# Performance work log

Hardware: AMD Instinct MI355X
Metric: run time of the kernel (lower is better)

## Reference

```python
import jax, jax.numpy as jnp
import numpy as np

NEG_INF = -1e6

def setup_inputs() -> dict:
    key = jax.random.key(0)
    ks = jax.random.split(key, 7)
    B, Q, K, D, H = 16, 64, 1024, 256, 128
    return {
        "queries": jax.random.normal(ks[0], (B, Q, D), dtype=jnp.float32),
        "keys": jax.random.normal(ks[1], (B, K, D), dtype=jnp.float32),
        "values": jax.random.normal(ks[2], (B, K, D), dtype=jnp.float32),
        "valid_lens": jax.random.randint(ks[3], (B,), 1, K + 1, dtype=jnp.int32),
        "W_q": jax.random.normal(ks[4], (D, H), dtype=jnp.float32) * (1.0 / np.sqrt(D)),
        "W_k": jax.random.normal(ks[5], (D, H), dtype=jnp.float32) * (1.0 / np.sqrt(D)),
        "w_v": jax.random.normal(ks[6], (H,), dtype=jnp.float32) * (1.0 / np.sqrt(H)),
    }

def reference(queries, keys, values, valid_lens, W_q, W_k, w_v):
    # project: [B,Q,H], [B,K,H]
    q = jnp.einsum('bqd,dh->bqh', queries, W_q)
    k = jnp.einsum('bkd,dh->bkh', keys, W_k)
    # broadcast add -> tanh -> score: [B,Q,K]
    features = jnp.tanh(q[:, :, None, :] + k[:, None, :, :])  # [B,Q,K,H]
    scores = jnp.einsum('bqkh,h->bqk', features, w_v)
    # masked softmax over key axis (valid_lens per batch)
    K_len = keys.shape[1]
    mask = jnp.arange(K_len)[None, None, :] < valid_lens[:, None, None]  # [B,1,K]
    scores = jnp.where(mask, scores, NEG_INF)
    attn = jax.nn.softmax(scores, axis=-1)
    # weighted sum of values: [B,Q,Dv]  (dropout p=0 -> identity)
    return jnp.einsum('bqk,bkd->bqd', attn, values)
```

## Files before the change

kernel.cpp:

```cpp
#include <hip/hip_runtime.h>

#define DDIM 256
#define HDIM 128
#define KLEN 1024
#define SCL 2.8853900817779268f

__global__ __launch_bounds__(256) void proj_kernel(
    const float* __restrict__ queries, const float* __restrict__ keys,
    const float* __restrict__ W_q, const float* __restrict__ W_k,
    float* __restrict__ Eq, float* __restrict__ Ek)
{
    __shared__ union {
        float a[64 * 64];
        float t[32][68];
    } sm;

    const int tid  = threadIdx.x;
    const int lane = tid & 63;
    const int wav  = tid >> 6;

    int blk = blockIdx.x;
    bool iskey; int b = 0, kc0 = 0, hb, row0;
    const float* in; const float* W;
    if (blk < 1024) {
        iskey = true;
        int xcd = blk & 7, s = blk >> 3;
        b = ((s >> 6) << 3) | xcd;
        int r6 = s & 63;
        kc0 = (r6 >> 2) << 6;
        hb  = (r6 & 3) << 5;
        row0 = b * KLEN + kc0;
        in = keys; W = W_k;
    } else {
        iskey = false;
        int qrb = blk - 1024;
        row0 = (qrb >> 2) << 6;
        hb   = (qrb & 3) << 5;
        in = queries; W = W_q;
    }

    const int hg8 = __builtin_amdgcn_readfirstlane(wav << 3);
    const float* Wu = W + hb + hg8;

    const int srow = tid >> 4;
    const int sgd  = tid & 15;
    const float* gsrc = in + (size_t)(row0 + srow) * DDIM + (sgd << 2);

    float4 pf0 = *(const float4*)(gsrc);
    float4 pf1 = *(const float4*)(gsrc + 16 * DDIM);
    float4 pf2 = *(const float4*)(gsrc + 32 * DDIM);
    float4 pf3 = *(const float4*)(gsrc + 48 * DDIM);

    float acc[8];
    #pragma unroll
    for (int c = 0; c < 8; c++) acc[c] = 0.f;

    const int w0 = (srow)      * 64 + ((sgd ^ ((srow)      & 7)) << 2);
    const int w1 = (srow + 16) * 64 + ((sgd ^ ((srow + 16) & 7)) << 2);
    const int w2 = (srow + 32) * 64 + ((sgd ^ ((srow + 32) & 7)) << 2);
    const int w3 = (srow + 48) * 64 + ((sgd ^ ((srow + 48) & 7)) << 2);

    for (int dt0 = 0; dt0 < DDIM; dt0 += 64) {
        *(float4*)(sm.a + w0) = pf0;
        *(float4*)(sm.a + w1) = pf1;
        *(float4*)(sm.a + w2) = pf2;
        *(float4*)(sm.a + w3) = pf3;
        __syncthreads();
        if (dt0 < DDIM - 64) {
            const float* g2 = gsrc + dt0 + 64;
            pf0 = *(const float4*)(g2);
            pf1 = *(const float4*)(g2 + 16 * DDIM);
            pf2 = *(const float4*)(g2 + 32 * DDIM);
            pf3 = *(const float4*)(g2 + 48 * DDIM);
        }
        const float* arow = sm.a + lane * 64;
        const int lx = lane & 7;
        #pragma unroll
        for (int d4 = 0; d4 < 64; d4 += 4) {
            float4 a = *(const float4*)(arow + ((((d4 >> 2)) ^ lx) << 2));
            const float* wr = Wu + (size_t)(dt0 + d4) * HDIM;
            #pragma unroll
            for (int c = 0; c < 8; c++) acc[c] = fmaf(a.x, wr[c],            acc[c]);
            #pragma unroll
            for (int c = 0; c < 8; c++) acc[c] = fmaf(a.y, wr[HDIM + c],     acc[c]);
            #pragma unroll
            for (int c = 0; c < 8; c++) acc[c] = fmaf(a.z, wr[2 * HDIM + c], acc[c]);
            #pragma unroll
            for (int c = 0; c < 8; c++) acc[c] = fmaf(a.w, wr[3 * HDIM + c], acc[c]);
        }
        __syncthreads();
    }

    float e[8];
    #pragma unroll
    for (int c = 0; c < 8; c++) e[c] = __builtin_amdgcn_exp2f(SCL * acc[c]);

    if (!iskey) {
        float* dst = Eq + (size_t)(row0 + lane) * HDIM + hb + hg8;
        *(float4*)(dst)     = make_float4(e[0], e[1], e[2], e[3]);
        *(float4*)(dst + 4) = make_float4(e[4], e[5], e[6], e[7]);
    } else {
        #pragma unroll
        for (int c = 0; c < 8; c++) sm.t[(wav << 3) + c][lane] = e[c];
        __syncthreads();
        float* dstb = Ek + (size_t)b * HDIM * KLEN + (size_t)hb * KLEN + kc0;
        #pragma unroll
        for (int i = 0; i < 2; i++) {
            int g = tid + (i << 8);
            int h = g >> 4, k4 = (g & 15) << 2;
            float4 o = *(const float4*)(&sm.t[h][k4]);
            *(float4*)(dstb + (size_t)h * KLEN + k4) = o;
        }
    }
}

__global__ __launch_bounds__(256) void score_kernel(
    const float* __restrict__ Eq, const float* __restrict__ Ek,
    const float* __restrict__ w_v, const int* __restrict__ valid_lens,
    float* __restrict__ E)
{
    __shared__ float ekt[16][128];
    __shared__ float eqs[8][HDIM];
    __shared__ float w2s[HDIM];

    const int tid = threadIdx.x;
    const int lane = tid & 63, wav = tid >> 6;
    int blk = blockIdx.x;
    int xcd = blk & 7, s = blk >> 3;
    int b = ((s >> 6) << 3) | xcd;
    int r = s & 63;
    int qt = r >> 3, kq = r & 7;
    int bq0 = b * 64 + qt * 8;
    int k0g = kq << 7;

    if (tid < HDIM) w2s[tid] = -2.0f * w_v[tid];
    #pragma unroll
    for (int i = 0; i < 4; i++) {
        int slot = tid + (i << 8);
        int q = slot >> 7, h = slot & 127;
        eqs[q][h] = Eq[(size_t)(bq0 + q) * HDIM + h];
    }

    const float* ekb = Ek + (size_t)b * HDIM * KLEN + k0g;
    float4 pf[2];
    #pragma unroll
    for (int i = 0; i < 2; i++) {
        int slot = tid + (i << 8);
        int row = slot >> 5, g = slot & 31;
        pf[i] = *(const float4*)(ekb + (size_t)row * KLEN + (g << 2));
    }

    const int q0 = wav << 1;
    const int kl = lane << 1;
    float2 acc[2] = {make_float2(0.f, 0.f), make_float2(0.f, 0.f)};

    for (int c = 0; c < 8; c++) {
        __syncthreads();
        #pragma unroll
        for (int i = 0; i < 2; i++) {
            int slot = tid + (i << 8);
            int row = slot >> 5, g = slot & 31;
            *(float4*)(&ekt[row][g << 2]) = pf[i];
        }
        __syncthreads();
        if (c < 7) {
            const float* nx = ekb + (size_t)((c + 1) << 4) * KLEN;
            #pragma unroll
            for (int i = 0; i < 2; i++) {
                int slot = tid + (i << 8);
                int row = slot >> 5, g = slot & 31;
                pf[i] = *(const float4*)(nx + (size_t)row * KLEN + (g << 2));
            }
        }
        const int c16 = c << 4;
        #pragma unroll
        for (int h4 = 0; h4 < 16; h4 += 4) {
            float4 eqa = *(const float4*)(&eqs[q0][c16 + h4]);
            float4 eqb = *(const float4*)(&eqs[q0 + 1][c16 + h4]);
            float4 w2v = *(const float4*)(&w2s[c16 + h4]);
            float ea[4] = {eqa.x, eqa.y, eqa.z, eqa.w};
            float eb[4] = {eqb.x, eqb.y, eqb.z, eqb.w};
            float wv[4] = {w2v.x, w2v.y, w2v.z, w2v.w};
            #pragma unroll
            for (int hh = 0; hh < 4; hh++) {
                float2 ek = *(const float2*)(&ekt[h4 + hh][kl]);
                float w2 = wv[hh];
                acc[0].x = fmaf(w2, __builtin_amdgcn_rcpf(fmaf(ea[hh], ek.x, 1.f)), acc[0].x);
                acc[0].y = fmaf(w2, __builtin_amdgcn_rcpf(fmaf(ea[hh], ek.y, 1.f)), acc[0].y);
                acc[1].x = fmaf(w2, __builtin_amdgcn_rcpf(fmaf(eb[hh], ek.x, 1.f)), acc[1].x);
                acc[1].y = fmaf(w2, __builtin_amdgcn_rcpf(fmaf(eb[hh], ek.y, 1.f)), acc[1].y);
            }
        }
    }

    int vlen = valid_lens[b];
    int kg = k0g + kl;
    #pragma unroll
    for (int j = 0; j < 2; j++) {
        float2 ev;
        ev.x = (kg     < vlen) ? __expf(acc[j].x) : 0.f;
        ev.y = (kg + 1 < vlen) ? __expf(acc[j].y) : 0.f;
        *(float2*)(E + (size_t)(bq0 + q0 + j) * KLEN + kg) = ev;
    }
}

__global__ __launch_bounds__(256) void av_kernel(
    const float* __restrict__ E, const float* __restrict__ values,
    const int* __restrict__ valid_lens, float* __restrict__ part,
    float* __restrict__ Tp)
{
    __shared__ union {
        float  pt[512][8];
        float4 slab[4][8][64];
    } sm;
    __shared__ float tslab[4][8];

    int blk = blockIdx.x;
    int xcd = blk & 7, s = blk >> 3;
    int b = ((s >> 4) << 3) | xcd;
    int r = s & 15, qt = r >> 1, kh = r & 1;
    int tid = threadIdx.x, lane = tid & 63, w = tid >> 6;
    int vlen = valid_lens[b];
    int bq0 = b * 64 + qt * 8;
    int kbase = kh << 9;

    #pragma unroll
    for (int i = 0; i < 4; i++) {
        int slot = tid + (i << 8);
        int q = slot >> 7, k4 = (slot & 127) << 2;
        float4 pv = *(const float4*)(E + (size_t)(bq0 + q) * KLEN + kbase + k4);
        sm.pt[k4 + 0][q] = pv.x;
        sm.pt[k4 + 1][q] = pv.y;
        sm.pt[k4 + 2][q] = pv.z;
        sm.pt[k4 + 3][q] = pv.w;
    }
    __syncthreads();

    int kw = w << 7;
    int cnt = vlen - (kbase + kw); cnt = cnt < 0 ? 0 : (cnt > 128 ? 128 : cnt);
    int cnt4 = (cnt + 3) & ~3;
    const float* vb = values + ((size_t)b * KLEN + kbase + kw) * DDIM + (lane << 2);

    float4 acc[8];
    float acct[8];
    #pragma unroll
    for (int q = 0; q < 8; q++) { acc[q] = make_float4(0.f, 0.f, 0.f, 0.f); acct[q] = 0.f; }

    for (int k = 0; k < cnt4; k += 4) {
        #pragma unroll
        for (int j = 0; j < 4; j++) {
            float4 v  = *(const float4*)(vb + (size_t)(k + j) * DDIM);
            float4 p0 = *(const float4*)(&sm.pt[kw + k + j][0]);
            float4 p1 = *(const float4*)(&sm.pt[kw + k + j][4]);
            float pq[8] = {p0.x, p0.y, p0.z, p0.w, p1.x, p1.y, p1.z, p1.w};
            #pragma unroll
            for (int q = 0; q < 8; q++) {
                acc[q].x = fmaf(pq[q], v.x, acc[q].x);
                acc[q].y = fmaf(pq[q], v.y, acc[q].y);
                acc[q].z = fmaf(pq[q], v.z, acc[q].z);
                acc[q].w = fmaf(pq[q], v.w, acc[q].w);
                acct[q] += pq[q];
            }
        }
    }

    __syncthreads();
    #pragma unroll
    for (int q = 0; q < 8; q++) sm.slab[w][q][lane] = acc[q];
    if (lane == 0) {
        #pragma unroll
        for (int q = 0; q < 8; q++) tslab[w][q] = acct[q];
    }
    __syncthreads();
    #pragma unroll
    for (int e = 0; e < 2; e++) {
        int slot = (tid << 1) | e;
        int q = slot >> 6, d4 = slot & 63;
        float4 a = sm.slab[0][q][d4];
        #pragma unroll
        for (int g = 1; g < 4; g++) {
            float4 t = sm.slab[g][q][d4];
            a.x += t.x; a.y += t.y; a.z += t.z; a.w += t.w;
        }
        *(float4*)(part + ((size_t)kh * 1024 + bq0 + q) * DDIM + (d4 << 2)) = a;
    }
    if (tid < 8) {
        float t = tslab[0][tid] + tslab[1][tid] + tslab[2][tid] + tslab[3][tid];
        Tp[(size_t)kh * 1024 + bq0 + tid] = t;
    }
}

__global__ __launch_bounds__(256) void combine_kernel(
    const float* __restrict__ part, const float* __restrict__ Tp,
    float* __restrict__ out)
{
    int i = blockIdx.x * 256 + threadIdx.x;
    int row = i >> 6;
    const float4* p4 = (const float4*)part;
    float4 a = p4[i];
    float4 v = p4[65536 + i];
    float inv = 1.0f / (Tp[row] + Tp[1024 + row]);
    a.x = (a.x + v.x) * inv; a.y = (a.y + v.y) * inv;
    a.z = (a.z + v.z) * inv; a.w = (a.w + v.w) * inv;
    ((float4*)out)[i] = a;
}

extern "C" void kernel_launch(void* const* d_in, const int* in_sizes, int n_in,
                              void* d_out, int out_size, void* d_ws, size_t ws_size,
                              hipStream_t stream) {
    const float* queries    = (const float*)d_in[0];
    const float* keys       = (const float*)d_in[1];
    const float* values     = (const float*)d_in[2];
    const int*   valid_lens = (const int*)d_in[3];
    const float* W_q        = (const float*)d_in[4];
    const float* W_k        = (const float*)d_in[5];
    const float* w_v        = (const float*)d_in[6];

    float* Eq   = (float*)d_ws;
    float* Ek   = Eq + 131072;
    float* E    = Ek + 2097152;
    float* Tp   = E + 1048576;
    float* part = Ek;

    proj_kernel<<<1088, 256, 0, stream>>>(queries, keys, W_q, W_k, Eq, Ek);
    score_kernel<<<1024, 256, 0, stream>>>(Eq, Ek, w_v, valid_lens, E);
    av_kernel<<<256, 256, 0, stream>>>(E, values, valid_lens, part, Tp);
    combine_kernel<<<256, 256, 0, stream>>>(part, Tp, (float*)d_out);
}
```

Baseline: 154.7 us.

## Fuse score and attention-value kernels, split key axis into eight partials

Merges the score kernel and the AV kernel into one kernel. Each block computes exp-scores for its 8 queries × 128 keys, keeps them in shared memory, and immediately accumulates the weighted values for that key chunk. This removes the global round trip of the score matrix E and one kernel launch. Ek is now read straight from global memory through a register double buffer instead of being staged in shared memory. The split-K factor grows from 2 to 8, so the combine kernel now reduces 8 partial outputs and 8 partial sums, which adds partial-buffer traffic.

```diff
diff --git a/kernel.cpp b/kernel.cpp
--- a/kernel.cpp
+++ b/kernel.cpp
@@ -114,14 +114,20 @@
     }
 }
 
-__global__ __launch_bounds__(256) void score_kernel(
+__global__ __launch_bounds__(256) void score_av_kernel(
     const float* __restrict__ Eq, const float* __restrict__ Ek,
     const float* __restrict__ w_v, const int* __restrict__ valid_lens,
-    float* __restrict__ E)
+    const float* __restrict__ values,
+    float* __restrict__ part, float* __restrict__ Tp)
 {
-    __shared__ float ekt[16][128];
-    __shared__ float eqs[8][HDIM];
-    __shared__ float w2s[HDIM];
+    __shared__ union {
+        struct {
+            float4 eqw[4][HDIM];
+            float  el[128][8];
+        } p;
+        float4 slab[4][8][64];
+    } sm;
+    __shared__ float tslab[4][8];
 
     const int tid = threadIdx.x;
     const int lane = tid & 63, wav = tid >> 6;
@@ -132,114 +138,63 @@
     int qt = r >> 3, kq = r & 7;
     int bq0 = b * 64 + qt * 8;
     int k0g = kq << 7;
-
-    if (tid < HDIM) w2s[tid] = -2.0f * w_v[tid];
-    #pragma unroll
-    for (int i = 0; i < 4; i++) {
-        int slot = tid + (i << 8);
-        int q = slot >> 7, h = slot & 127;
-        eqs[q][h] = Eq[(size_t)(bq0 + q) * HDIM + h];
-    }
-
-    const float* ekb = Ek + (size_t)b * HDIM * KLEN + k0g;
-    float4 pf[2];
+    int vlen = valid_lens[b];
+
     #pragma unroll
     for (int i = 0; i < 2; i++) {
         int slot = tid + (i << 8);
-        int row = slot >> 5, g = slot & 31;
-        pf[i] = *(const float4*)(ekb + (size_t)row * KLEN + (g << 2));
-    }
-
-    const int q0 = wav << 1;
+        int w = slot >> 7, h = slot & 127;
+        sm.p.eqw[w][h] = make_float4(
+            Eq[(size_t)(bq0 + 2 * w) * HDIM + h],
+            Eq[(size_t)(bq0 + 2 * w + 1) * HDIM + h],
+            -2.0f * w_v[h], 0.f);
+    }
+    __syncthreads();
+
     const int kl = lane << 1;
-    float2 acc[2] = {make_float2(0.f, 0.f), make_float2(0.f, 0.f)};
-
-    for (int c = 0; c < 8; c++) {
-        __syncthreads();
-        #pragma unroll
-        for (int i = 0; i < 2; i++) {
-            int slot = tid + (i << 8);
-            int row = slot >> 5, g = slot & 31;
-            *(float4*)(&ekt[row][g << 2]) = pf[i];
-        }
-        __syncthreads();
-        if (c < 7) {
-            const float* nx = ekb + (size_t)((c + 1) << 4) * KLEN;
-            #pragma unroll
-            for (int i = 0; i < 2; i++) {
-                int slot = tid + (i << 8);
-                int row = slot >> 5, g = slot & 31;
-                pf[i] = *(const float4*)(nx + (size_t)row * KLEN + (g << 2));
-            }
-        }
-        const int c16 = c << 4;
-        #pragma unroll
-        for (int h4 = 0; h4 < 16; h4 += 4) {
-            float4 eqa = *(const float4*)(&eqs[q0][c16 + h4]);
-            float4 eqb = *(const float4*)(&eqs[q0 + 1][c16 + h4]);
-            float4 w2v = *(const float4*)(&w2s[c16 + h4]);
-            float ea[4] = {eqa.x, eqa.y, eqa.z, eqa.w};
-            float eb[4] = {eqb.x, eqb.y, eqb.z, eqb.w};
-            float wv[4] = {w2v.x, w2v.y, w2v.z, w2v.w};
-            #pragma unroll
-            for (int hh = 0; hh < 4; hh++) {
-                float2 ek = *(const float2*)(&ekt[h4 + hh][kl]);
-                float w2 = wv[hh];
-                acc[0].x = fmaf(w2, __builtin_amdgcn_rcpf(fmaf(ea[hh], ek.x, 1.f)), acc[0].x);
-                acc[0].y = fmaf(w2, __builtin_amdgcn_rcpf(fmaf(ea[hh], ek.y, 1.f)), acc[0].y);
-                acc[1].x = fmaf(w2, __builtin_amdgcn_rcpf(fmaf(eb[hh], ek.x, 1.f)), acc[1].x);
-                acc[1].y = fmaf(w2, __builtin_amdgcn_rcpf(fmaf(eb[hh], ek.y, 1.f)), acc[1].y);
-            }
-        }
-    }
-
-    int vlen = valid_lens[b];
-    int kg = k0g + kl;
-    #pragma unroll
-    for (int j = 0; j < 2; j++) {
-        float2 ev;
-        ev.x = (kg     < vlen) ? __expf(acc[j].x) : 0.f;
-        ev.y = (kg + 1 < vlen) ? __expf(acc[j].y) : 0.f;
-        *(float2*)(E + (size_t)(bq0 + q0 + j) * KLEN + kg) = ev;
-    }
-}
-
-__global__ __launch_bounds__(256) void av_kernel(
-    const float* __restrict__ E, const float* __restrict__ values,
-    const int* __restrict__ valid_lens, float* __restrict__ part,
-    float* __restrict__ Tp)
-{
-    __shared__ union {
-        float  pt[512][8];
-        float4 slab[4][8][64];
-    } sm;
-    __shared__ float tslab[4][8];
-
-    int blk = blockIdx.x;
-    int xcd = blk & 7, s = blk >> 3;
-    int b = ((s >> 4) << 3) | xcd;
-    int r = s & 15, qt = r >> 1, kh = r & 1;
-    int tid = threadIdx.x, lane = tid & 63, w = tid >> 6;
-    int vlen = valid_lens[b];
-    int bq0 = b * 64 + qt * 8;
-    int kbase = kh << 9;
-
-    #pragma unroll
-    for (int i = 0; i < 4; i++) {
-        int slot = tid + (i << 8);
-        int q = slot >> 7, k4 = (slot & 127) << 2;
-        float4 pv = *(const float4*)(E + (size_t)(bq0 + q) * KLEN + kbase + k4);
-        sm.pt[k4 + 0][q] = pv.x;
-        sm.pt[k4 + 1][q] = pv.y;
-        sm.pt[k4 + 2][q] = pv.z;
-        sm.pt[k4 + 3][q] = pv.w;
-    }
-    __syncthreads();
-
-    int kw = w << 7;
-    int cnt = vlen - (kbase + kw); cnt = cnt < 0 ? 0 : (cnt > 128 ? 128 : cnt);
+    const float* ekp = Ek + (size_t)b * HDIM * KLEN + k0g + kl;
+    float2 buf[8];
+    #pragma unroll
+    for (int j = 0; j < 8; j++)
+        buf[j] = *(const float2*)(ekp + (size_t)j * KLEN);
+
+    float2 acc0 = make_float2(0.f, 0.f), acc1 = make_float2(0.f, 0.f);
+    for (int h0 = 0; h0 < HDIM; h0 += 8) {
+        float2 nxt[8];
+        if (h0 < HDIM - 8) {
+            #pragma unroll
+            for (int j = 0; j < 8; j++)
+                nxt[j] = *(const float2*)(ekp + (size_t)(h0 + 8 + j) * KLEN);
+        }
+        #pragma unroll
+        for (int j = 0; j < 8; j++) {
+            float4 e = sm.p.eqw[wav][h0 + j];
+            float2 ek = buf[j];
+            acc0.x = fmaf(e.z, __builtin_amdgcn_rcpf(fmaf(e.x, ek.x, 1.f)), acc0.x);
+            acc0.y = fmaf(e.z, __builtin_amdgcn_rcpf(fmaf(e.x, ek.y, 1.f)), acc0.y);
+            acc1.x = fmaf(e.z, __builtin_amdgcn_rcpf(fmaf(e.y, ek.x, 1.f)), acc1.x);
+            acc1.y = fmaf(e.z, __builtin_amdgcn_rcpf(fmaf(e.y, ek.y, 1.f)), acc1.y);
+        }
+        #pragma unroll
+        for (int j = 0; j < 8; j++) buf[j] = nxt[j];
+    }
+
+    {
+        int kg = k0g + kl;
+        float e00 = (kg     < vlen) ? __expf(acc0.x) : 0.f;
+        float e01 = (kg + 1 < vlen) ? __expf(acc0.y) : 0.f;
+        float e10 = (kg     < vlen) ? __expf(acc1.x) : 0.f;
+        float e11 = (kg + 1 < vlen) ? __expf(acc1.y) : 0.f;
+        *(float2*)(&sm.p.el[kl][2 * wav])     = make_float2(e00, e10);
+        *(float2*)(&sm.p.el[kl + 1][2 * wav]) = make_float2(e01, e11);
+    }
+    __syncthreads();
+
+    int kw = wav << 5;
+    int kg0 = k0g + kw;
+    int cnt = vlen - kg0; cnt = cnt < 0 ? 0 : (cnt > 32 ? 32 : cnt);
     int cnt4 = (cnt + 3) & ~3;
-    const float* vb = values + ((size_t)b * KLEN + kbase + kw) * DDIM + (lane << 2);
+    const float* vb = values + ((size_t)b * KLEN + kg0) * DDIM + (lane << 2);
 
     float4 acc[8];
     float acct[8];
@@ -250,8 +205,8 @@
         #pragma unroll
         for (int j = 0; j < 4; j++) {
             float4 v  = *(const float4*)(vb + (size_t)(k + j) * DDIM);
-            float4 p0 = *(const float4*)(&sm.pt[kw + k + j][0]);
-            float4 p1 = *(const float4*)(&sm.pt[kw + k + j][4]);
+            float4 p0 = *(const float4*)(&sm.p.el[kw + k + j][0]);
+            float4 p1 = *(const float4*)(&sm.p.el[kw + k + j][4]);
             float pq[8] = {p0.x, p0.y, p0.z, p0.w, p1.x, p1.y, p1.z, p1.w};
             #pragma unroll
             for (int q = 0; q < 8; q++) {
@@ -266,10 +221,10 @@
 
     __syncthreads();
     #pragma unroll
-    for (int q = 0; q < 8; q++) sm.slab[w][q][lane] = acc[q];
+    for (int q = 0; q < 8; q++) sm.slab[wav][q][lane] = acc[q];
     if (lane == 0) {
         #pragma unroll
-        for (int q = 0; q < 8; q++) tslab[w][q] = acct[q];
+        for (int q = 0; q < 8; q++) tslab[wav][q] = acct[q];
     }
     __syncthreads();
     #pragma unroll
@@ -282,11 +237,11 @@
             float4 t = sm.slab[g][q][d4];
             a.x += t.x; a.y += t.y; a.z += t.z; a.w += t.w;
         }
-        *(float4*)(part + ((size_t)kh * 1024 + bq0 + q) * DDIM + (d4 << 2)) = a;
+        *(float4*)(part + ((size_t)kq * 1024 + bq0 + q) * DDIM + (d4 << 2)) = a;
     }
     if (tid < 8) {
         float t = tslab[0][tid] + tslab[1][tid] + tslab[2][tid] + tslab[3][tid];
-        Tp[(size_t)kh * 1024 + bq0 + tid] = t;
+        Tp[(size_t)kq * 1024 + bq0 + tid] = t;
     }
 }
 
@@ -297,11 +252,17 @@
     int i = blockIdx.x * 256 + threadIdx.x;
     int row = i >> 6;
     const float4* p4 = (const float4*)part;
+    float t = 0.f;
+    #pragma unroll
+    for (int j = 0; j < 8; j++) t += Tp[(size_t)j * 1024 + row];
+    float inv = 1.0f / t;
     float4 a = p4[i];
-    float4 v = p4[65536 + i];
-    float inv = 1.0f / (Tp[row] + Tp[1024 + row]);
-    a.x = (a.x + v.x) * inv; a.y = (a.y + v.y) * inv;
-    a.z = (a.z + v.z) * inv; a.w = (a.w + v.w) * inv;
+    #pragma unroll
+    for (int j = 1; j < 8; j++) {
+        float4 v = p4[(size_t)j * 65536 + i];
+        a.x += v.x; a.y += v.y; a.z += v.z; a.w += v.w;
+    }
+    a.x *= inv; a.y *= inv; a.z *= inv; a.w *= inv;
     ((float4*)out)[i] = a;
 }
 
@@ -318,12 +279,10 @@
 
     float* Eq   = (float*)d_ws;
     float* Ek   = Eq + 131072;
-    float* E    = Ek + 2097152;
-    float* Tp   = E + 1048576;
-    float* part = Ek;
+    float* part = Ek + 2097152;
+    float* Tp   = part + 2097152;
 
     proj_kernel<<<1088, 256, 0, stream>>>(queries, keys, W_q, W_k, Eq, Ek);
-    score_kernel<<<1024, 256, 0, stream>>>(Eq, Ek, w_v, valid_lens, E);
-    av_kernel<<<256, 256, 0, stream>>>(E, values, valid_lens, part, Tp);
+    score_av_kernel<<<1024, 256, 0, stream>>>(Eq, Ek, w_v, valid_lens, values, part, Tp);
     combine_kernel<<<256, 256, 0, stream>>>(part, Tp, (float*)d_out);
 }
```

Measured after the change: 136.2 us, median of 2. 1.14x faster.
